# Kernel optimization log

Hardware: AMD Instinct MI355X
Metric: run time of the kernel (lower is better)

## Reference

```python
import jax, jax.numpy as jnp
import numpy as np

B, T, C, H = 2, 2048, 1024, 16
HD = C // H  # head dim = 64


def setup_inputs() -> dict:
    key = jax.random.key(0)
    k1, k2, k3 = jax.random.split(key, 3)
    x = jax.random.normal(k1, (B, T, C), dtype=jnp.float32)
    W_attn = jax.random.normal(k2, (C, 3 * C), dtype=jnp.float32) * (C ** -0.5)
    W_proj = jax.random.normal(k3, (C, C), dtype=jnp.float32) * (C ** -0.5)
    b_proj = jnp.zeros((C,), dtype=jnp.float32)
    return {"x": x, "W_attn": W_attn, "W_proj": W_proj, "b_proj": b_proj}


def reference(x, W_attn, W_proj, b_proj):
    Bv, Tv, Cv = x.shape
    qkv = x @ W_attn  # [B, T, 3C]  (no bias: config.bias=False)
    # NOTE: source splits as k, q, v (k first!)
    k, q, v = jnp.split(qkv, 3, axis=2)
    # [B, H, T, HD]
    q = q.reshape(Bv, Tv, H, HD).transpose(0, 2, 1, 3)
    k = k.reshape(Bv, Tv, H, HD).transpose(0, 2, 1, 3)
    v = v.reshape(Bv, Tv, H, HD).transpose(0, 2, 1, 3)
    wei = jnp.einsum('bhqd,bhkd->bhqk', q, k) * (HD ** -0.5)
    causal = jnp.tril(jnp.ones((Tv, Tv), dtype=bool))
    wei = jnp.where(causal, wei, -jnp.inf)
    wei = jax.nn.softmax(wei, axis=-1)
    # dropout = 0.0 (eval) -> identity
    out = jnp.einsum('bhqk,bhkd->bhqd', wei, v)
    out = out.transpose(0, 2, 1, 3).reshape(Bv, Tv, Cv)
    out = out @ W_proj + b_proj
    return out
```

## Files before the change

kernel.cpp:

```cpp
#include <hip/hip_runtime.h>

typedef __attribute__((ext_vector_type(8))) short short8;
typedef __attribute__((ext_vector_type(4))) short short4v;
typedef __attribute__((ext_vector_type(4))) float float4v;

#define T_SEQ 2048
#define CDIM 1024
#define NHEAD 16
#define HDIM 64
#define PROW 72

__device__ __forceinline__ unsigned short f2bf(float f) {
    unsigned u = __builtin_bit_cast(unsigned, f);
    u += 0x7FFF + ((u >> 16) & 1);
    return (unsigned short)(u >> 16);
}

__device__ __forceinline__ void gload16(const unsigned short* g,
                                        unsigned short* l) {
    __builtin_amdgcn_global_load_lds(
        (const __attribute__((address_space(1))) unsigned int*)g,
        (__attribute__((address_space(3))) unsigned int*)l, 16, 0, 0);
}

__device__ __forceinline__ void phase_barrier() {
    __builtin_amdgcn_sched_barrier(0);
    __builtin_amdgcn_s_barrier();
    __builtin_amdgcn_sched_barrier(0);
}

__global__ __launch_bounds__(256) void preproc(
    const float* __restrict__ x, unsigned short* __restrict__ xb,
    const float* __restrict__ Wa, unsigned short* __restrict__ WaT,
    const float* __restrict__ Wp, unsigned short* __restrict__ WpT) {
    int bid = blockIdx.x, tid = threadIdx.x;
    if (bid < 4096) {
        int i = bid * 256 + tid;
        float4 v = ((const float4*)x)[i];
        ushort4 o;
        o.x = f2bf(v.x); o.y = f2bf(v.y); o.z = f2bf(v.z); o.w = f2bf(v.w);
        ((ushort4*)xb)[i] = o;
        return;
    }
    __shared__ float tile[32][33];
    const float* in;
    unsigned short* out;
    int N, b;
    if (bid < 4096 + 3072) {
        b = bid - 4096; in = Wa; out = WaT; N = 3072;
    } else {
        b = bid - 7168; in = Wp; out = WpT; N = 1024;
    }
    const int K = 1024;
    int kb = (b & 31) * 32, nb = (b >> 5) * 32;
    int tx = tid & 31, ty = tid >> 5;
    for (int r = 0; r < 4; r++)
        tile[ty + r * 8][tx] = in[(size_t)(kb + ty + r * 8) * N + nb + tx];
    __syncthreads();
    for (int r = 0; r < 4; r++)
        out[(size_t)(nb + ty + r * 8) * K + kb + tx] = f2bf(tile[tx][ty + r * 8]);
}

__global__ __launch_bounds__(256) void gemm_qkv(
    const unsigned short* __restrict__ A, const unsigned short* __restrict__ Bt,
    unsigned short* __restrict__ dK, unsigned short* __restrict__ dQ,
    unsigned short* __restrict__ dV) {
    const int K = 1024;
    const int NITER = K / 32;
    __shared__ unsigned short sA[3][128 * 32];
    __shared__ unsigned short sB[3][128 * 32];
    int tid = threadIdx.x, wave = tid >> 6, lane = tid & 63;
    int quad = lane >> 4, l16 = lane & 15;
    int wm = wave >> 1, wn = wave & 1;
    int blockM = blockIdx.y * 128, blockN = blockIdx.x * 128;
    bool swapAB = (blockN >= 2048);

    const unsigned short* gA = A + (size_t)blockM * K;
    const unsigned short* gB = Bt + (size_t)blockN * K;

    int srow = wave * 32 + (lane >> 2);
    int scol = (lane & 3) * 8;
    const unsigned short* pa0 = gA + (size_t)srow * K + scol;
    const unsigned short* pa1 = pa0 + (size_t)16 * K;
    const unsigned short* pb0 = gB + (size_t)srow * K + scol;
    const unsigned short* pb1 = pb0 + (size_t)16 * K;
    int lo0 = (wave * 32) * 32;
    int lo1 = (wave * 32 + 16) * 32;

    float4v acc[4][4] = {};
    int aoff = (wm * 64 + l16) * 32 + quad * 8;
    int boff = (wn * 64 + l16) * 32 + quad * 8;

    for (int t = 0; t < 2; t++) {
        int kb = t * 32;
        gload16(pa0 + kb, sA[t] + lo0);
        gload16(pa1 + kb, sA[t] + lo1);
        gload16(pb0 + kb, sB[t] + lo0);
        gload16(pb1 + kb, sB[t] + lo1);
    }
    asm volatile("s_waitcnt vmcnt(4)" ::: "memory");
    phase_barrier();

#pragma unroll
    for (int it = 0; it < NITER; it++) {
        int cur = it % 3;
        if (it + 2 < NITER) {
            int kb = (it + 2) * 32;
            int nb = (it + 2) % 3;
            gload16(pa0 + kb, sA[nb] + lo0);
            gload16(pa1 + kb, sA[nb] + lo1);
            gload16(pb0 + kb, sB[nb] + lo0);
            gload16(pb1 + kb, sB[nb] + lo1);
        }
        const unsigned short* cA = sA[cur];
        const unsigned short* cB = sB[cur];
        short8 af[4], bf[4];
        for (int i = 0; i < 4; i++)
            af[i] = *(const short8*)(cA + aoff + i * 16 * 32);
        for (int j = 0; j < 4; j++)
            bf[j] = *(const short8*)(cB + boff + j * 16 * 32);
        if (!swapAB) {
            for (int i = 0; i < 4; i++)
                for (int j = 0; j < 4; j++)
                    acc[i][j] = __builtin_amdgcn_mfma_f32_16x16x32_bf16(
                        af[i], bf[j], acc[i][j], 0, 0, 0);
        } else {
            for (int i = 0; i < 4; i++)
                for (int j = 0; j < 4; j++)
                    acc[i][j] = __builtin_amdgcn_mfma_f32_16x16x32_bf16(
                        bf[j], af[i], acc[i][j], 0, 0, 0);
        }
        if (it + 1 < NITER) {
            if (it + 2 < NITER) {
                asm volatile("s_waitcnt vmcnt(4)" ::: "memory");
            } else {
                asm volatile("s_waitcnt vmcnt(0)" ::: "memory");
            }
            phase_barrier();
        }
    }

    if (!swapAB) {
        const float QSCL = 0.18033688011112042f;
        for (int i = 0; i < 4; i++)
            for (int j = 0; j < 4; j++)
                for (int r = 0; r < 4; r++) {
                    int m = blockM + wm * 64 + i * 16 + quad * 4 + r;
                    int n = blockN + wn * 64 + j * 16 + l16;
                    int part = n >> 10, c = n & 1023;
                    int h = c >> 6, d = c & 63;
                    int bb = m >> 11, t = m & 2047;
                    int bh = bb * NHEAD + h;
                    if (part == 0) {
                        dK[(((size_t)bh * T_SEQ + t) << 6) + d] = f2bf(acc[i][j][r]);
                    } else {
                        dQ[(((size_t)bh * T_SEQ + t) << 6) + d] =
                            f2bf(acc[i][j][r] * QSCL);
                    }
                }
    } else {
        for (int i = 0; i < 4; i++)
            for (int j = 0; j < 4; j++)
                for (int r = 0; r < 4; r++) {
                    int n = blockN + wn * 64 + j * 16 + quad * 4 + r;
                    int m = blockM + wm * 64 + i * 16 + l16;
                    int c = n & 1023;
                    int h = c >> 6, d = c & 63;
                    int bb = m >> 11, t = m & 2047;
                    int bh = bb * NHEAD + h;
                    dV[((size_t)bh * HDIM + d) * T_SEQ + t] = f2bf(acc[i][j][r]);
                }
    }
}

__global__ __launch_bounds__(256) void gemm_proj(
    const unsigned short* __restrict__ A, const unsigned short* __restrict__ Bt,
    const float* __restrict__ bias, float* __restrict__ out) {
    const int K = 1024;
    const int NITER = K / 64;
    __shared__ unsigned short sA[2][64 * PROW];
    __shared__ unsigned short sB[2][64 * PROW];
    int tid = threadIdx.x, wave = tid >> 6, lane = tid & 63;
    int quad = lane >> 4, l16 = lane & 15;
    int wm = wave >> 1, wn = wave & 1;
    int blockM = blockIdx.y * 64, blockN = blockIdx.x * 64;

    int srow = tid >> 3;
    int sseg = tid & 7;
    const unsigned short* gA0 = A + (size_t)(blockM + srow) * K + sseg * 8;
    const unsigned short* gA1 = gA0 + (size_t)32 * K;
    const unsigned short* gB0 = Bt + (size_t)(blockN + srow) * K + sseg * 8;
    const unsigned short* gB1 = gB0 + (size_t)32 * K;
    int so0 = srow * PROW + sseg * 8;
    int so1 = (srow + 32) * PROW + sseg * 8;

    float4v acc[2][2] = {};
    uint4 ra0, ra1, rb0, rb1;

    ra0 = *(const uint4*)gA0; ra1 = *(const uint4*)gA1;
    rb0 = *(const uint4*)gB0; rb1 = *(const uint4*)gB1;
    *(uint4*)(sA[0] + so0) = ra0;
    *(uint4*)(sA[0] + so1) = ra1;
    *(uint4*)(sB[0] + so0) = rb0;
    *(uint4*)(sB[0] + so1) = rb1;

    int aoff = (wm * 32 + l16) * PROW + quad * 8;
    int boff = (wn * 32 + l16) * PROW + quad * 8;

    for (int it = 0; it < NITER; it++) {
        int cur = it & 1;
        __syncthreads();
        if (it + 1 < NITER) {
            int kb = (it + 1) * 64;
            ra0 = *(const uint4*)(gA0 + kb); ra1 = *(const uint4*)(gA1 + kb);
            rb0 = *(const uint4*)(gB0 + kb); rb1 = *(const uint4*)(gB1 + kb);
        }
        const unsigned short* cA = sA[cur];
        const unsigned short* cB = sB[cur];
        short8 af[2][2], bf[2][2];
        for (int i = 0; i < 2; i++)
            for (int k = 0; k < 2; k++)
                af[i][k] = *(const short8*)(cA + aoff + i * 16 * PROW + k * 32);
        for (int j = 0; j < 2; j++)
            for (int k = 0; k < 2; k++)
                bf[j][k] = *(const short8*)(cB + boff + j * 16 * PROW + k * 32);
        for (int i = 0; i < 2; i++)
            for (int j = 0; j < 2; j++) {
                acc[i][j] = __builtin_amdgcn_mfma_f32_16x16x32_bf16(
                    af[i][0], bf[j][0], acc[i][j], 0, 0, 0);
                acc[i][j] = __builtin_amdgcn_mfma_f32_16x16x32_bf16(
                    af[i][1], bf[j][1], acc[i][j], 0, 0, 0);
            }
        if (it + 1 < NITER) {
            int nxt = cur ^ 1;
            *(uint4*)(sA[nxt] + so0) = ra0;
            *(uint4*)(sA[nxt] + so1) = ra1;
            *(uint4*)(sB[nxt] + so0) = rb0;
            *(uint4*)(sB[nxt] + so1) = rb1;
        }
    }

    for (int i = 0; i < 2; i++)
        for (int j = 0; j < 2; j++)
            for (int r = 0; r < 4; r++) {
                int m = blockM + wm * 32 + i * 16 + quad * 4 + r;
                int n = blockN + wn * 32 + j * 16 + l16;
                out[(size_t)m * CDIM + n] = acc[i][j][r] + bias[n];
            }
}

__global__ __launch_bounds__(256) void attn_fwd(
    const unsigned short* __restrict__ Qp, const unsigned short* __restrict__ Kp,
    const unsigned short* __restrict__ Vt, unsigned short* __restrict__ att) {
    __shared__ unsigned short sK[2][64 * 72];
    __shared__ unsigned short sV[2][64 * 72];
    int tid = threadIdx.x, wave = tid >> 6, lane = tid & 63;
    int quad = lane >> 4, l16 = lane & 15;
    int bh = blockIdx.x;
    int bb = bh >> 4, h = bh & 15;
    size_t baseQ = (size_t)bh * T_SEQ * HDIM;
    size_t baseV = (size_t)bh * HDIM * T_SEQ;
    int row4 = tid >> 2, seg = tid & 3;

    int xt = 31 - blockIdx.y;
    int qb = xt * 64;
    int qrow = qb + wave * 16 + l16;

    const unsigned short* qr = Qp + baseQ + (size_t)qrow * HDIM;
    short8 qf0 = *(const short8*)(qr + quad * 8);
    short8 qf1 = *(const short8*)(qr + 32 + quad * 8);

    float4v o[4] = {};
    float lsum = 0.f;
    int nt = xt + 1;

    uint4 ka, kb2, va, vb;
    {
        const unsigned short* gk = Kp + baseQ + (size_t)row4 * HDIM + seg * 16;
        const unsigned short* gv = Vt + baseV + (size_t)row4 * T_SEQ + seg * 16;
        ka = *(const uint4*)gk; kb2 = *(const uint4*)(gk + 8);
        va = *(const uint4*)gv; vb = *(const uint4*)(gv + 8);
    }
    *(uint4*)(sK[0] + row4 * 72 + seg * 16) = ka;
    *(uint4*)(sK[0] + row4 * 72 + seg * 16 + 8) = kb2;
    *(uint4*)(sV[0] + row4 * 72 + seg * 16) = va;
    *(uint4*)(sV[0] + row4 * 72 + seg * 16 + 8) = vb;

    const float4v NEG16 = {-16.f, -16.f, -16.f, -16.f};

    for (int t = 0; t < nt; t++) {
        int cur = t & 1;
        __syncthreads();
        if (t + 1 < nt) {
            const unsigned short* gk =
                Kp + baseQ + (size_t)((t + 1) * 64 + row4) * HDIM + seg * 16;
            const unsigned short* gv =
                Vt + baseV + (size_t)row4 * T_SEQ + (t + 1) * 64 + seg * 16;
            ka = *(const uint4*)gk; kb2 = *(const uint4*)(gk + 8);
            va = *(const uint4*)gv; vb = *(const uint4*)(gv + 8);
        }

        const unsigned short* cK = sK[cur];
        const unsigned short* cV = sV[cur];
        float4v s[4];
        __builtin_amdgcn_s_setprio(1);
        for (int sub = 0; sub < 4; sub++) {
            short8 kf0 = *(const short8*)(cK + (sub * 16 + l16) * 72 + quad * 8);
            short8 kf1 =
                *(const short8*)(cK + (sub * 16 + l16) * 72 + 32 + quad * 8);
            float4v z = NEG16;
            z = __builtin_amdgcn_mfma_f32_16x16x32_bf16(kf0, qf0, z, 0, 0, 0);
            z = __builtin_amdgcn_mfma_f32_16x16x32_bf16(kf1, qf1, z, 0, 0, 0);
            s[sub] = z;
        }
        __builtin_amdgcn_s_setprio(0);

        float e[16];
        bool need_mask = (t * 64 + 63) > (qb + wave * 16);
        if (need_mask) {
            int kgb = t * 64 + quad * 4;
            for (int sub = 0; sub < 4; sub++)
                for (int r = 0; r < 4; r++) {
                    float v = __builtin_amdgcn_exp2f(s[sub][r]);
                    v = (kgb + sub * 16 + r <= qrow) ? v : 0.0f;
                    e[sub * 4 + r] = v;
                    lsum += v;
                }
        } else {
            for (int sub = 0; sub < 4; sub++)
                for (int r = 0; r < 4; r++) {
                    float v = __builtin_amdgcn_exp2f(s[sub][r]);
                    e[sub * 4 + r] = v;
                    lsum += v;
                }
        }

        __builtin_amdgcn_s_setprio(1);
        for (int sub = 0; sub < 4; sub++) {
            unsigned lo, hi;
            asm("v_cvt_pk_bf16_f32 %0, %1, %2"
                : "=v"(lo) : "v"(e[sub * 4 + 0]), "v"(e[sub * 4 + 1]));
            asm("v_cvt_pk_bf16_f32 %0, %1, %2"
                : "=v"(hi) : "v"(e[sub * 4 + 2]), "v"(e[sub * 4 + 3]));
            uint2 packed = {lo, hi};
            short4v pf = __builtin_bit_cast(short4v, packed);
            for (int dc = 0; dc < 4; dc++) {
                short4v vf = *(const short4v*)(
                    cV + (dc * 16 + l16) * 72 + sub * 16 + quad * 4);
                o[dc] = __builtin_amdgcn_mfma_f32_16x16x16bf16_1k(
                    vf, pf, o[dc], 0, 0, 0);
            }
        }
        __builtin_amdgcn_s_setprio(0);

        if (t + 1 < nt) {
            int nxt = cur ^ 1;
            *(uint4*)(sK[nxt] + row4 * 72 + seg * 16) = ka;
            *(uint4*)(sK[nxt] + row4 * 72 + seg * 16 + 8) = kb2;
            *(uint4*)(sV[nxt] + row4 * 72 + seg * 16) = va;
            *(uint4*)(sV[nxt] + row4 * 72 + seg * 16 + 8) = vb;
        }
    }

    lsum += __shfl_xor(lsum, 16);
    lsum += __shfl_xor(lsum, 32);
    float inv = 1.0f / lsum;

    __syncthreads();
    for (int dc = 0; dc < 4; dc++) {
        short4v ov;
        for (int r = 0; r < 4; r++) ov[r] = (short)f2bf(o[dc][r] * inv);
        *(short4v*)(sK[0] + wave * 1152 + l16 * 72 + dc * 16 + quad * 4) = ov;
    }
    __syncthreads();
    int orow = lane >> 2, oseg = lane & 3;
    uint4 a = *(const uint4*)(sK[0] + wave * 1152 + orow * 72 + oseg * 16);
    uint4 b = *(const uint4*)(sK[0] + wave * 1152 + orow * 72 + oseg * 16 + 8);
    unsigned short* dst = att +
        (size_t)(bb * T_SEQ + qb + wave * 16 + orow) * CDIM + h * HDIM +
        oseg * 16;
    *(uint4*)dst = a;
    *(uint4*)(dst + 8) = b;
}

extern "C" void kernel_launch(void* const* d_in, const int* in_sizes, int n_in,
                              void* d_out, int out_size, void* d_ws, size_t ws_size,
                              hipStream_t stream) {
    const float* x      = (const float*)d_in[0];
    const float* W_attn = (const float*)d_in[1];
    const float* W_proj = (const float*)d_in[2];
    const float* b_proj = (const float*)d_in[3];
    float* out = (float*)d_out;

    unsigned short* xb   = (unsigned short*)d_ws;
    unsigned short* WaT  = xb  + 4096 * 1024;
    unsigned short* WpT  = WaT + 3072 * 1024;
    unsigned short* Karr = WpT + 1024 * 1024;
    unsigned short* Qarr = Karr + 2 * 16 * 2048 * 64;
    unsigned short* Varr = Qarr + 2 * 16 * 2048 * 64;
    unsigned short* attb = Varr + 2 * 16 * 2048 * 64;

    preproc<<<8192, 256, 0, stream>>>(x, xb, W_attn, WaT, W_proj, WpT);
    gemm_qkv<<<dim3(24, 32), 256, 0, stream>>>(xb, WaT, Karr, Qarr, Varr);
    attn_fwd<<<dim3(32, 32), 256, 0, stream>>>(Qarr, Karr, Varr, attb);
    gemm_proj<<<dim3(16, 64), 256, 0, stream>>>(attb, WpT, b_proj, out);
}
```

Before: 187.3 us.

## Enlarge QKV GEMM tile to 256x256 with 8 waves and interleaved prefetch schedule

Reworks the QKV projection GEMM to use 256x256 block tiles with 512 threads, a K-step of 64 and double-buffered LDS, in place of 128x128 tiles with a triple buffer. Each K-step is split into four MFMA quarters, with A and B global-to-LDS prefetches interleaved between them and s_setprio raised around the MFMA bursts. The goal is more operand reuse per loaded byte and better overlap of loads with matrix math. The cost is 128 KB of LDS, one block per CU, many barriers per K-step, and a grid of only 192 blocks, which may not fill the device.

```diff
diff --git a/kernel.cpp b/kernel.cpp
--- a/kernel.cpp
+++ b/kernel.cpp
@@ -61,114 +61,147 @@
         out[(size_t)(nb + ty + r * 8) * K + kb + tx] = f2bf(tile[tx][ty + r * 8]);
 }
 
-__global__ __launch_bounds__(256) void gemm_qkv(
+__global__ __launch_bounds__(512, 1) void gemm_qkv(
     const unsigned short* __restrict__ A, const unsigned short* __restrict__ Bt,
     unsigned short* __restrict__ dK, unsigned short* __restrict__ dQ,
     unsigned short* __restrict__ dV) {
     const int K = 1024;
-    const int NITER = K / 32;
-    __shared__ unsigned short sA[3][128 * 32];
-    __shared__ unsigned short sB[3][128 * 32];
+    const int NT = K / 64;
+    __shared__ unsigned short sA[2][256 * 64];
+    __shared__ unsigned short sB[2][256 * 64];
     int tid = threadIdx.x, wave = tid >> 6, lane = tid & 63;
     int quad = lane >> 4, l16 = lane & 15;
-    int wm = wave >> 1, wn = wave & 1;
-    int blockM = blockIdx.y * 128, blockN = blockIdx.x * 128;
+    int wm = wave >> 2, wn = wave & 3;
+    int blockM = blockIdx.y * 256, blockN = blockIdx.x * 256;
     bool swapAB = (blockN >= 2048);
 
     const unsigned short* gA = A + (size_t)blockM * K;
     const unsigned short* gB = Bt + (size_t)blockN * K;
 
-    int srow = wave * 32 + (lane >> 2);
-    int scol = (lane & 3) * 8;
-    const unsigned short* pa0 = gA + (size_t)srow * K + scol;
-    const unsigned short* pa1 = pa0 + (size_t)16 * K;
-    const unsigned short* pb0 = gB + (size_t)srow * K + scol;
-    const unsigned short* pb1 = pb0 + (size_t)16 * K;
-    int lo0 = (wave * 32) * 32;
-    int lo1 = (wave * 32 + 16) * 32;
-
-    float4v acc[4][4] = {};
-    int aoff = (wm * 64 + l16) * 32 + quad * 8;
-    int boff = (wn * 64 + l16) * 32 + quad * 8;
-
-    for (int t = 0; t < 2; t++) {
-        int kb = t * 32;
-        gload16(pa0 + kb, sA[t] + lo0);
-        gload16(pa1 + kb, sA[t] + lo1);
-        gload16(pb0 + kb, sB[t] + lo0);
-        gload16(pb1 + kb, sB[t] + lo1);
-    }
-    asm volatile("s_waitcnt vmcnt(4)" ::: "memory");
+    int r0 = (wave * 2) * 8 + (lane >> 3);
+    int r1 = (wave * 2 + 1) * 8 + (lane >> 3);
+    int scol = (lane & 7) * 8;
+    int lds_c0 = (wave * 2) * 8 * 64;
+    int lds_c1 = (wave * 2 + 1) * 8 * 64;
+
+#define STAGE_HALF(sX, gX, d, h, kt)                                          \
+    do {                                                                      \
+        gload16(gX + (size_t)((h)*128 + r0) * K + (kt)*64 + scol,             \
+                &sX[d][(h)*128 * 64 + lds_c0]);                               \
+        gload16(gX + (size_t)((h)*128 + r1) * K + (kt)*64 + scol,             \
+                &sX[d][(h)*128 * 64 + lds_c1]);                               \
+    } while (0)
+
+    float4v acc[8][4] = {};
+    int aoff = (wm * 128 + l16) * 64 + quad * 8;
+    int boff = (wn * 64 + l16) * 64 + quad * 8;
+
+    STAGE_HALF(sA, gA, 0, 0, 0);
+    STAGE_HALF(sA, gA, 0, 1, 0);
+    STAGE_HALF(sB, gB, 0, 0, 0);
+    STAGE_HALF(sB, gB, 0, 1, 0);
+    asm volatile("s_waitcnt vmcnt(0)" ::: "memory");
     phase_barrier();
 
-#pragma unroll
-    for (int it = 0; it < NITER; it++) {
-        int cur = it % 3;
-        if (it + 2 < NITER) {
-            int kb = (it + 2) * 32;
-            int nb = (it + 2) % 3;
-            gload16(pa0 + kb, sA[nb] + lo0);
-            gload16(pa1 + kb, sA[nb] + lo1);
-            gload16(pb0 + kb, sB[nb] + lo0);
-            gload16(pb1 + kb, sB[nb] + lo1);
-        }
-        const unsigned short* cA = sA[cur];
-        const unsigned short* cB = sB[cur];
-        short8 af[4], bf[4];
-        for (int i = 0; i < 4; i++)
-            af[i] = *(const short8*)(cA + aoff + i * 16 * 32);
+#define MFMA_QUAD(q)                                                          \
+    do {                                                                      \
+        __builtin_amdgcn_s_setprio(1);                                        \
+        for (int i = 0; i < 2; i++)                                           \
+            for (int j = 0; j < 4; j++)                                       \
+                for (int ks = 0; ks < 2; ks++)                                \
+                    acc[(q)*2 + i][j] =                                       \
+                        swapAB ? __builtin_amdgcn_mfma_f32_16x16x32_bf16(     \
+                                     bf[j][ks], af[i][ks], acc[(q)*2 + i][j], \
+                                     0, 0, 0)                                 \
+                               : __builtin_amdgcn_mfma_f32_16x16x32_bf16(     \
+                                     af[i][ks], bf[j][ks], acc[(q)*2 + i][j], \
+                                     0, 0, 0);                                \
+        __builtin_amdgcn_s_setprio(0);                                        \
+    } while (0)
+
+#pragma unroll 2
+    for (int kt = 0; kt < NT; kt++) {
+        int d = kt & 1;
+        const unsigned short* cA = sA[d];
+        const unsigned short* cB = sB[d];
+        short8 bf[4][2], af[2][2];
         for (int j = 0; j < 4; j++)
-            bf[j] = *(const short8*)(cB + boff + j * 16 * 32);
-        if (!swapAB) {
-            for (int i = 0; i < 4; i++)
-                for (int j = 0; j < 4; j++)
-                    acc[i][j] = __builtin_amdgcn_mfma_f32_16x16x32_bf16(
-                        af[i], bf[j], acc[i][j], 0, 0, 0);
-        } else {
-            for (int i = 0; i < 4; i++)
-                for (int j = 0; j < 4; j++)
-                    acc[i][j] = __builtin_amdgcn_mfma_f32_16x16x32_bf16(
-                        bf[j], af[i], acc[i][j], 0, 0, 0);
-        }
-        if (it + 1 < NITER) {
-            if (it + 2 < NITER) {
-                asm volatile("s_waitcnt vmcnt(4)" ::: "memory");
-            } else {
-                asm volatile("s_waitcnt vmcnt(0)" ::: "memory");
-            }
-            phase_barrier();
-        }
-    }
+            for (int ks = 0; ks < 2; ks++)
+                bf[j][ks] = *(const short8*)(cB + boff + j * 16 * 64 + ks * 32);
+        for (int i = 0; i < 2; i++)
+            for (int ks = 0; ks < 2; ks++)
+                af[i][ks] = *(const short8*)(cA + aoff + i * 16 * 64 + ks * 32);
+        if (kt + 1 < NT) {
+            STAGE_HALF(sA, gA, d ^ 1, 0, kt + 1);
+            STAGE_HALF(sA, gA, d ^ 1, 1, kt + 1);
+        }
+        phase_barrier();
+        asm volatile("s_waitcnt lgkmcnt(0)" ::: "memory");
+        __builtin_amdgcn_sched_barrier(0);
+        MFMA_QUAD(0);
+        phase_barrier();
+        for (int i = 0; i < 2; i++)
+            for (int ks = 0; ks < 2; ks++)
+                af[i][ks] = *(const short8*)(cA + aoff + (2 + i) * 16 * 64 + ks * 32);
+        if (kt + 1 < NT) {
+            STAGE_HALF(sB, gB, d ^ 1, 0, kt + 1);
+            STAGE_HALF(sB, gB, d ^ 1, 1, kt + 1);
+        }
+        phase_barrier();
+        asm volatile("s_waitcnt lgkmcnt(0)" ::: "memory");
+        __builtin_amdgcn_sched_barrier(0);
+        MFMA_QUAD(1);
+        phase_barrier();
+        for (int i = 0; i < 2; i++)
+            for (int ks = 0; ks < 2; ks++)
+                af[i][ks] = *(const short8*)(cA + aoff + (4 + i) * 16 * 64 + ks * 32);
+        phase_barrier();
+        asm volatile("s_waitcnt lgkmcnt(0)" ::: "memory");
+        __builtin_amdgcn_sched_barrier(0);
+        MFMA_QUAD(2);
+        phase_barrier();
+        for (int i = 0; i < 2; i++)
+            for (int ks = 0; ks < 2; ks++)
+                af[i][ks] = *(const short8*)(cA + aoff + (6 + i) * 16 * 64 + ks * 32);
+        phase_barrier();
+        asm volatile("s_waitcnt lgkmcnt(0)" ::: "memory");
+        __builtin_amdgcn_sched_barrier(0);
+        MFMA_QUAD(3);
+        asm volatile("s_waitcnt vmcnt(0)" ::: "memory");
+        phase_barrier();
+    }
+#undef MFMA_QUAD
+#undef STAGE_HALF
 
     if (!swapAB) {
         const float QSCL = 0.18033688011112042f;
-        for (int i = 0; i < 4; i++)
+        for (int i = 0; i < 8; i++)
             for (int j = 0; j < 4; j++)
                 for (int r = 0; r < 4; r++) {
-                    int m = blockM + wm * 64 + i * 16 + quad * 4 + r;
+                    int m = blockM + wm * 128 + i * 16 + quad * 4 + r;
                     int n = blockN + wn * 64 + j * 16 + l16;
                     int part = n >> 10, c = n & 1023;
-                    int h = c >> 6, d = c & 63;
+                    int h = c >> 6, dd = c & 63;
                     int bb = m >> 11, t = m & 2047;
                     int bh = bb * NHEAD + h;
                     if (part == 0) {
-                        dK[(((size_t)bh * T_SEQ + t) << 6) + d] = f2bf(acc[i][j][r]);
+                        dK[(((size_t)bh * T_SEQ + t) << 6) + dd] = f2bf(acc[i][j][r]);
                     } else {
-                        dQ[(((size_t)bh * T_SEQ + t) << 6) + d] =
+                        dQ[(((size_t)bh * T_SEQ + t) << 6) + dd] =
                             f2bf(acc[i][j][r] * QSCL);
                     }
                 }
     } else {
-        for (int i = 0; i < 4; i++)
+        for (int i = 0; i < 8; i++)
             for (int j = 0; j < 4; j++)
                 for (int r = 0; r < 4; r++) {
                     int n = blockN + wn * 64 + j * 16 + quad * 4 + r;
-                    int m = blockM + wm * 64 + i * 16 + l16;
+                    int m = blockM + wm * 128 + i * 16 + l16;
                     int c = n & 1023;
-                    int h = c >> 6, d = c & 63;
+                    int h = c >> 6, dd = c & 63;
                     int bb = m >> 11, t = m & 2047;
                     int bh = bb * NHEAD + h;
-                    dV[((size_t)bh * HDIM + d) * T_SEQ + t] = f2bf(acc[i][j][r]);
+                    dV[((size_t)bh * HDIM + dd) * T_SEQ + t] = f2bf(acc[i][j][r]);
                 }
     }
 }
@@ -401,7 +434,7 @@
     unsigned short* attb = Varr + 2 * 16 * 2048 * 64;
 
     preproc<<<8192, 256, 0, stream>>>(x, xb, W_attn, WaT, W_proj, WpT);
-    gemm_qkv<<<dim3(24, 32), 256, 0, stream>>>(xb, WaT, Karr, Qarr, Varr);
+    gemm_qkv<<<dim3(12, 16), 512, 0, stream>>>(xb, WaT, Karr, Qarr, Varr);
     attn_fwd<<<dim3(32, 32), 256, 0, stream>>>(Qarr, Karr, Varr, attb);
     gemm_proj<<<dim3(16, 64), 256, 0, stream>>>(attb, WpT, b_proj, out);
 }
```

Result: slower. 206.8 us (+10.4%).

## Pipeline output projection GEMM with async LDS loads and triple buffering

Applied to the files above, without the earlier changes.

Rewrites the projection GEMM to load tiles straight into LDS with global_load_lds, using a three-stage ring buffer with a prefetch distance of two in place of register-staged double buffering. The N tile grows from 64 to 128, so each wave computes 32x64 and the grid is halved. The aim is to hide global load latency and raise MFMA work per barrier. In exchange, the unpadded 64-wide LDS rows may cause bank conflicts on the fragment reads, and fewer blocks are launched.

```diff
diff --git a/kernel.cpp b/kernel.cpp
--- a/kernel.cpp
+++ b/kernel.cpp
@@ -8,7 +8,6 @@
 #define CDIM 1024
 #define NHEAD 16
 #define HDIM 64
-#define PROW 72
 
 __device__ __forceinline__ unsigned short f2bf(float f) {
     unsigned u = __builtin_bit_cast(unsigned, f);
@@ -178,74 +177,94 @@
     const float* __restrict__ bias, float* __restrict__ out) {
     const int K = 1024;
     const int NITER = K / 64;
-    __shared__ unsigned short sA[2][64 * PROW];
-    __shared__ unsigned short sB[2][64 * PROW];
+    __shared__ unsigned short sA[3][64 * 64];
+    __shared__ unsigned short sB[3][128 * 64];
     int tid = threadIdx.x, wave = tid >> 6, lane = tid & 63;
     int quad = lane >> 4, l16 = lane & 15;
     int wm = wave >> 1, wn = wave & 1;
-    int blockM = blockIdx.y * 64, blockN = blockIdx.x * 64;
-
-    int srow = tid >> 3;
-    int sseg = tid & 7;
-    const unsigned short* gA0 = A + (size_t)(blockM + srow) * K + sseg * 8;
-    const unsigned short* gA1 = gA0 + (size_t)32 * K;
-    const unsigned short* gB0 = Bt + (size_t)(blockN + srow) * K + sseg * 8;
-    const unsigned short* gB1 = gB0 + (size_t)32 * K;
-    int so0 = srow * PROW + sseg * 8;
-    int so1 = (srow + 32) * PROW + sseg * 8;
-
-    float4v acc[2][2] = {};
-    uint4 ra0, ra1, rb0, rb1;
-
-    ra0 = *(const uint4*)gA0; ra1 = *(const uint4*)gA1;
-    rb0 = *(const uint4*)gB0; rb1 = *(const uint4*)gB1;
-    *(uint4*)(sA[0] + so0) = ra0;
-    *(uint4*)(sA[0] + so1) = ra1;
-    *(uint4*)(sB[0] + so0) = rb0;
-    *(uint4*)(sB[0] + so1) = rb1;
-
-    int aoff = (wm * 32 + l16) * PROW + quad * 8;
-    int boff = (wn * 32 + l16) * PROW + quad * 8;
-
+    int blockM = blockIdx.y * 64, blockN = blockIdx.x * 128;
+
+    const unsigned short* gA = A + (size_t)blockM * K;
+    const unsigned short* gB = Bt + (size_t)blockN * K;
+
+    int lr = lane >> 3;
+    int scol = (lane & 7) * 8;
+    const unsigned short* pa0 = gA + (size_t)((wave * 2 + 0) * 8 + lr) * K + scol;
+    const unsigned short* pa1 = gA + (size_t)((wave * 2 + 1) * 8 + lr) * K + scol;
+    const unsigned short* pb0 = gB + (size_t)((wave * 4 + 0) * 8 + lr) * K + scol;
+    const unsigned short* pb1 = gB + (size_t)((wave * 4 + 1) * 8 + lr) * K + scol;
+    const unsigned short* pb2 = gB + (size_t)((wave * 4 + 2) * 8 + lr) * K + scol;
+    const unsigned short* pb3 = gB + (size_t)((wave * 4 + 3) * 8 + lr) * K + scol;
+    int la0 = (wave * 2 + 0) * 8 * 64;
+    int la1 = (wave * 2 + 1) * 8 * 64;
+    int lb0 = (wave * 4 + 0) * 8 * 64;
+    int lb1 = (wave * 4 + 1) * 8 * 64;
+    int lb2 = (wave * 4 + 2) * 8 * 64;
+    int lb3 = (wave * 4 + 3) * 8 * 64;
+
+    float4v acc[2][4] = {};
+    int aoff = (wm * 32 + l16) * 64 + quad * 8;
+    int boff = (wn * 64 + l16) * 64 + quad * 8;
+
+    for (int t = 0; t < 2; t++) {
+        int kb = t * 64;
+        gload16(pa0 + kb, sA[t] + la0);
+        gload16(pa1 + kb, sA[t] + la1);
+        gload16(pb0 + kb, sB[t] + lb0);
+        gload16(pb1 + kb, sB[t] + lb1);
+        gload16(pb2 + kb, sB[t] + lb2);
+        gload16(pb3 + kb, sB[t] + lb3);
+    }
+    asm volatile("s_waitcnt vmcnt(6)" ::: "memory");
+    phase_barrier();
+
+#pragma unroll
     for (int it = 0; it < NITER; it++) {
-        int cur = it & 1;
-        __syncthreads();
-        if (it + 1 < NITER) {
-            int kb = (it + 1) * 64;
-            ra0 = *(const uint4*)(gA0 + kb); ra1 = *(const uint4*)(gA1 + kb);
-            rb0 = *(const uint4*)(gB0 + kb); rb1 = *(const uint4*)(gB1 + kb);
+        int cur = it % 3;
+        if (it + 2 < NITER) {
+            int kb = (it + 2) * 64;
+            int nb = (it + 2) % 3;
+            gload16(pa0 + kb, sA[nb] + la0);
+            gload16(pa1 + kb, sA[nb] + la1);
+            gload16(pb0 + kb, sB[nb] + lb0);
+            gload16(pb1 + kb, sB[nb] + lb1);
+            gload16(pb2 + kb, sB[nb] + lb2);
+            gload16(pb3 + kb, sB[nb] + lb3);
         }
         const unsigned short* cA = sA[cur];
         const unsigned short* cB = sB[cur];
-        short8 af[2][2], bf[2][2];
+        short8 af[2][2], bf[4][2];
         for (int i = 0; i < 2; i++)
-            for (int k = 0; k < 2; k++)
-                af[i][k] = *(const short8*)(cA + aoff + i * 16 * PROW + k * 32);
-        for (int j = 0; j < 2; j++)
-            for (int k = 0; k < 2; k++)
-                bf[j][k] = *(const short8*)(cB + boff + j * 16 * PROW + k * 32);
+            for (int ks = 0; ks < 2; ks++)
+                af[i][ks] = *(const short8*)(cA + aoff + i * 16 * 64 + ks * 32);
+        for (int j = 0; j < 4; j++)
+            for (int ks = 0; ks < 2; ks++)
+                bf[j][ks] = *(const short8*)(cB + boff + j * 16 * 64 + ks * 32);
         for (int i = 0; i < 2; i++)
-            for (int j = 0; j < 2; j++) {
+            for (int j = 0; j < 4; j++) {
                 acc[i][j] = __builtin_amdgcn_mfma_f32_16x16x32_bf16(
                     af[i][0], bf[j][0], acc[i][j], 0, 0, 0);
                 acc[i][j] = __builtin_amdgcn_mfma_f32_16x16x32_bf16(
                     af[i][1], bf[j][1], acc[i][j], 0, 0, 0);
             }
         if (it + 1 < NITER) {
-            int nxt = cur ^ 1;
-            *(uint4*)(sA[nxt] + so0) = ra0;
-            *(uint4*)(sA[nxt] + so1) = ra1;
-            *(uint4*)(sB[nxt] + so0) = rb0;
-            *(uint4*)(sB[nxt] + so1) = rb1;
-        }
-    }
-
+            if (it + 2 < NITER) {
+                asm volatile("s_waitcnt vmcnt(6)" ::: "memory");
+            } else {
+                asm volatile("s_waitcnt vmcnt(0)" ::: "memory");
+            }
+            phase_barrier();
+        }
+    }
+
+    float bv[4];
+    for (int j = 0; j < 4; j++) bv[j] = bias[blockN + wn * 64 + j * 16 + l16];
     for (int i = 0; i < 2; i++)
-        for (int j = 0; j < 2; j++)
+        for (int j = 0; j < 4; j++)
             for (int r = 0; r < 4; r++) {
                 int m = blockM + wm * 32 + i * 16 + quad * 4 + r;
-                int n = blockN + wn * 32 + j * 16 + l16;
-                out[(size_t)m * CDIM + n] = acc[i][j][r] + bias[n];
+                int n = blockN + wn * 64 + j * 16 + l16;
+                out[(size_t)m * CDIM + n] = acc[i][j][r] + bv[j];
             }
 }
 
@@ -403,5 +422,5 @@
     preproc<<<8192, 256, 0, stream>>>(x, xb, W_attn, WaT, W_proj, WpT);
     gemm_qkv<<<dim3(24, 32), 256, 0, stream>>>(xb, WaT, Karr, Qarr, Varr);
     attn_fwd<<<dim3(32, 32), 256, 0, stream>>>(Qarr, Karr, Varr, attb);
-    gemm_proj<<<dim3(16, 64), 256, 0, stream>>>(attb, WpT, b_proj, out);
-}
+    gemm_proj<<<dim3(8, 64), 256, 0, stream>>>(attb, WpT, b_proj, out);
+}
```

Result: slower. 191.2 us (+2.1%).
